# Optimization experiments

Hardware: AMD Instinct MI355X
Metric: run time of the kernel (lower is better)

The kernel has to match this reference:

```python
import jax, jax.numpy as jnp
import numpy as np

B, S, D, H = 1, 2048, 2048, 32
HD = D // H  # head_dim = 64
FF = 4 * D
EPS = 1e-5


def _alibi_slopes(n_heads):
    # standard ALiBi slopes for power-of-2 head counts: 2^(-8i/n)
    return np.array([2.0 ** (-8.0 * (i + 1) / n_heads) for i in range(n_heads)], np.float32)


def setup_inputs() -> dict:
    key = jax.random.key(0)
    ks = jax.random.split(key, 16)
    s = 0.02
    x = jax.random.normal(ks[0], (B, S, D), jnp.float32)
    # alibi bias [B, H, 1, S], broadcast over query positions (HF views alibi as (b, h, 1, kv_len))
    slopes = _alibi_slopes(H)
    alibi_np = slopes[:, None, None] * np.arange(S, dtype=np.float32)[None, None, :]
    alibi = jnp.broadcast_to(jnp.asarray(alibi_np), (B, H, 1, S))
    # additive causal mask [1, 1, S, S]
    causal = np.tril(np.ones((S, S), bool))
    attention_mask = jnp.asarray(np.where(causal, 0.0, -1e9).astype(np.float32))[None, None]
    p = lambda k, shp: s * jax.random.normal(k, shp, jnp.float32)
    return {
        "x": x,
        "alibi": alibi,
        "attention_mask": attention_mask,
        "ln1_g": jnp.ones((D,), jnp.float32), "ln1_b": jnp.zeros((D,), jnp.float32),
        "ln2_g": jnp.ones((D,), jnp.float32), "ln2_b": jnp.zeros((D,), jnp.float32),
        "wqkv": p(ks[1], (D, 3 * D)), "bqkv": jnp.zeros((3 * D,), jnp.float32),
        "wo": p(ks[2], (D, D)), "bo": jnp.zeros((D,), jnp.float32),
        "w1": p(ks[3], (D, FF)), "b1": jnp.zeros((FF,), jnp.float32),
        "w2": p(ks[4], (FF, D)), "b2": jnp.zeros((D,), jnp.float32),
    }


def _layernorm(h, g, b):
    m = h.mean(-1, keepdims=True)
    v = ((h - m) ** 2).mean(-1, keepdims=True)
    return (h - m) * jax.lax.rsqrt(v + EPS) * g + b


def reference(x, alibi, attention_mask, ln1_g, ln1_b, ln2_g, ln2_b,
              wqkv, bqkv, wo, bo, w1, b1, w2, b2):
    b, s, d = x.shape
    inv_norm = 1.0 / np.sqrt(HD).astype(np.float32)
    # --- input layernorm ---
    h = _layernorm(x, ln1_g, ln1_b)
    # --- fused QKV ---
    qkv = h @ wqkv + bqkv
    q, k, v = jnp.split(qkv, 3, axis=-1)
    q = q.reshape(b, s, H, HD).transpose(0, 2, 1, 3)  # [b, h, s, hd]
    k = k.reshape(b, s, H, HD).transpose(0, 2, 1, 3)
    v = v.reshape(b, s, H, HD).transpose(0, 2, 1, 3)
    # --- ALiBi-biased attention (HF falcon alibi path) ---
    scores = jnp.einsum("bhqd,bhkd->bhqk", q, k)          # [b, h, s, s]
    logits = (scores + alibi) * inv_norm + attention_mask  # alibi broadcasts over q dim
    probs = jax.nn.softmax(logits, axis=-1)
    ctx = jnp.einsum("bhqk,bhkd->bhqd", probs, v)
    ctx = ctx.transpose(0, 2, 1, 3).reshape(b, s, d)
    attn_out = ctx @ wo + bo
    # --- residual, post-attn layernorm, MLP (non-parallel falcon-rw layout) ---
    res = x + attn_out
    h2 = _layernorm(res, ln2_g, ln2_b)
    mlp = jax.nn.gelu(h2 @ w1 + b1, approximate=False) @ w2 + b2
    return res + mlp
```

## Files before the change

### kernel.cpp

```cpp
#include <hip/hip_runtime.h>
#include <hip/hip_bf16.h>
#include <cstdint>
#include <cstddef>

static constexpr int Sq  = 2048;
static constexpr int Dm  = 2048;
static constexpr int NH  = 32;
static constexpr int HDm = 64;
static constexpr int FFm = 8192;

typedef __bf16 bf16x8 __attribute__((ext_vector_type(8)));
typedef float  f32x4  __attribute__((ext_vector_type(4)));

__device__ __forceinline__ void async_ld16(const void* g, void* l) {
  __builtin_amdgcn_global_load_lds((const __attribute__((address_space(1))) void*)g,
                                   (__attribute__((address_space(3))) void*)l, 16, 0, 0);
}

__global__ __launch_bounds__(256)
void tcast_kernel(const float* __restrict__ in, __hip_bfloat16* __restrict__ out,
                  int K, int N) {
  __shared__ float tile[64][65];
  const int tc = blockIdx.x * 64;
  const int tr = blockIdx.y * 64;
  const int cx = threadIdx.x & 63;
  const int ry = threadIdx.x >> 6;
#pragma unroll
  for (int i = 0; i < 16; ++i) {
    int r = ry + i * 4;
    tile[r][cx] = in[(size_t)(tr + r) * N + tc + cx];
  }
  __syncthreads();
#pragma unroll
  for (int i = 0; i < 16; ++i) {
    int r = ry + i * 4;
    out[(size_t)(tc + r) * K + tr + cx] = __float2bfloat16(tile[cx][r]);
  }
}

__global__ __launch_bounds__(256)
void ln_kernel(const float* __restrict__ x, const float* __restrict__ g,
               const float* __restrict__ b, __hip_bfloat16* __restrict__ out) {
  __shared__ float red[4];
  const int t = threadIdx.x;
  const float* xr = x + (size_t)blockIdx.x * Dm;
  float v[8];
  float s = 0.f;
#pragma unroll
  for (int i = 0; i < 8; ++i) { v[i] = xr[t + i * 256]; s += v[i]; }
#pragma unroll
  for (int off = 32; off > 0; off >>= 1) s += __shfl_down(s, off, 64);
  if ((t & 63) == 0) red[t >> 6] = s;
  __syncthreads();
  const float mean = (red[0] + red[1] + red[2] + red[3]) * (1.f / Dm);
  __syncthreads();
  float vs = 0.f;
#pragma unroll
  for (int i = 0; i < 8; ++i) { float d = v[i] - mean; vs += d * d; }
#pragma unroll
  for (int off = 32; off > 0; off >>= 1) vs += __shfl_down(vs, off, 64);
  if ((t & 63) == 0) red[t >> 6] = vs;
  __syncthreads();
  const float inv = rsqrtf((red[0] + red[1] + red[2] + red[3]) * (1.f / Dm) + 1e-5f);
  __hip_bfloat16* orow = out + (size_t)blockIdx.x * Dm;
#pragma unroll
  for (int i = 0; i < 8; ++i) {
    int c = t + i * 256;
    orow[c] = __float2bfloat16((v[i] - mean) * inv * g[c] + b[c]);
  }
}

template <int EPI>
__global__ __launch_bounds__(256)
void gemm_kernel(const __hip_bfloat16* __restrict__ A,
                 const __hip_bfloat16* __restrict__ Bt,
                 int N, int K, int Ksub,
                 const float* __restrict__ bias,
                 const float* __restrict__ addsrc,
                 float* __restrict__ outf,
                 __hip_bfloat16* __restrict__ outb,
                 __hip_bfloat16* __restrict__ qo,
                 __hip_bfloat16* __restrict__ ko,
                 __hip_bfloat16* __restrict__ vo,
                 __hip_bfloat16* __restrict__ po) {
  __shared__ __align__(16) __hip_bfloat16 As[2][128 * 32];
  __shared__ __align__(16) __hip_bfloat16 Bs[2][128 * 32];
  const int t = threadIdx.x;
  const int lane = t & 63, w = t >> 6, quad = lane >> 4, l16 = lane & 15;
  const int bn = blockIdx.x, bm = blockIdx.y, bz = blockIdx.z;
  const int wm = (w & 1) * 64, wn = (w >> 1) * 64;
  const __hip_bfloat16* Abase = A + (size_t)bm * 128 * K;
  const __hip_bfloat16* Bbase = Bt + (size_t)bn * 128 * K;
  const int kBeg = bz * Ksub, kEnd = kBeg + Ksub;

  auto stage = [&](int b, int k0) {
#pragma unroll
    for (int j = 0; j < 2; ++j) {
      int c = j * 256 + t;
      int row = c >> 2;
      int p = c & 3;
      int g = (p - (row >> 1)) & 3;
      async_ld16(Abase + (size_t)row * K + k0 + g * 8, &As[b][c * 8]);
      async_ld16(Bbase + (size_t)row * K + k0 + g * 8, &Bs[b][c * 8]);
    }
  };

  f32x4 acc[4][4] = {};
  stage(0, kBeg);
  int buf = 0;
  for (int k0 = kBeg; k0 < kEnd; k0 += 32, buf ^= 1) {
    __syncthreads();
    if (k0 + 32 < kEnd) stage(buf ^ 1, k0 + 32);
    bf16x8 af[4], bfv[4];
#pragma unroll
    for (int i = 0; i < 4; ++i) {
      int row = wm + i * 16 + l16;
      int p = (quad + (row >> 1)) & 3;
      af[i] = *(const bf16x8*)(&As[buf][row * 32 + p * 8]);
    }
#pragma unroll
    for (int i = 0; i < 4; ++i) {
      int row = wn + i * 16 + l16;
      int p = (quad + (row >> 1)) & 3;
      bfv[i] = *(const bf16x8*)(&Bs[buf][row * 32 + p * 8]);
    }
#pragma unroll
    for (int mt = 0; mt < 4; ++mt)
#pragma unroll
      for (int nt = 0; nt < 4; ++nt)
        acc[mt][nt] = __builtin_amdgcn_mfma_f32_16x16x32_bf16(af[mt], bfv[nt], acc[mt][nt], 0, 0, 0);
  }
#pragma unroll
  for (int mt = 0; mt < 4; ++mt) {
#pragma unroll
    for (int nt = 0; nt < 4; ++nt) {
      const int n = bn * 128 + wn + nt * 16 + l16;
      const float bz2 = bias[n];
#pragma unroll
      for (int r = 0; r < 4; ++r) {
        const int m = bm * 128 + wm + mt * 16 + quad * 4 + r;
        float val = acc[mt][nt][r];
        if constexpr (EPI == 0) {
          val += bz2;
          int which = n >> 11, d2 = n & 2047;
          int hh = d2 >> 6, hd = d2 & 63;
          if (which == 0)
            qo[((size_t)hh * Sq + m) * HDm + hd] = __float2bfloat16(val * 0.125f);
          else if (which == 1)
            ko[((size_t)hh * Sq + m) * HDm + hd] = __float2bfloat16(val);
          else
            vo[((size_t)hh * HDm + hd) * Sq + m] = __float2bfloat16(val);
        } else if constexpr (EPI == 1) {
          outf[(size_t)m * N + n] = addsrc[(size_t)m * N + n] + bz2 + val;
        } else if constexpr (EPI == 2) {
          val += bz2;
          float gg = 0.5f * val * (1.0f + erff(val * 0.70710678118654752f));
          outb[(size_t)m * N + n] = __float2bfloat16(gg);
        } else {
          if (bz == 0)
            outf[(size_t)m * N + n] = addsrc[(size_t)m * N + n] + bz2 + val;
          else
            po[(size_t)m * N + n] = __float2bfloat16(val);
        }
      }
    }
  }
}

__global__ __launch_bounds__(256)
void addp_kernel(float* __restrict__ out, const __hip_bfloat16* __restrict__ p) {
  const int i = (blockIdx.x * 256 + threadIdx.x) * 4;
  float4 o = *(const float4*)(out + i);
  const __hip_bfloat16* pp = p + i;
  o.x += (float)pp[0]; o.y += (float)pp[1]; o.z += (float)pp[2]; o.w += (float)pp[3];
  *(float4*)(out + i) = o;
}

__global__ __launch_bounds__(256)
void attn_kernel(const __hip_bfloat16* __restrict__ qb,
                 const __hip_bfloat16* __restrict__ kb,
                 const __hip_bfloat16* __restrict__ vt,
                 const float* __restrict__ alibi,
                 __hip_bfloat16* __restrict__ ctx) {
  __shared__ __align__(16) __hip_bfloat16 Kl[64 * 64];
  __shared__ __align__(16) __hip_bfloat16 Vl[64 * 64];
  __shared__ __align__(16) __hip_bfloat16 Pl[4][16 * 64];
  const int qblk = blockIdx.x, h = blockIdx.y;
  const int t = threadIdx.x, w = t >> 6, lane = t & 63, quad = lane >> 4, l16 = lane & 15;
  const __hip_bfloat16* qh = qb + (size_t)h * Sq * HDm;
  const __hip_bfloat16* kh = kb + (size_t)h * Sq * HDm;
  const __hip_bfloat16* vh = vt + (size_t)h * HDm * Sq;
  const float* al = alibi + (size_t)h * Sq;
  const int qr0 = qblk * 64 + w * 16;
  const bf16x8 qa0 = *(const bf16x8*)(qh + (size_t)(qr0 + l16) * HDm + quad * 8);
  const bf16x8 qa1 = *(const bf16x8*)(qh + (size_t)(qr0 + l16) * HDm + 32 + quad * 8);
  f32x4 o[4] = {};
  float m_i[4], l_i[4];
#pragma unroll
  for (int r = 0; r < 4; ++r) { m_i[r] = -3e38f; l_i[r] = 0.f; }
  for (int kbk = 0; kbk <= qblk; ++kbk) {
    __syncthreads();
#pragma unroll
    for (int j = 0; j < 2; ++j) {
      int c = j * 256 + t;
      int row = c >> 3;
      int swz = (c & 7) ^ (row & 7);
      async_ld16(kh + (size_t)(kbk * 64 + row) * HDm + swz * 8, Kl + c * 8);
      async_ld16(vh + (size_t)row * Sq + kbk * 64 + swz * 8, Vl + c * 8);
    }
    __syncthreads();
    f32x4 sf[4];
    const f32x4 zero = {};
#pragma unroll
    for (int nt = 0; nt < 4; ++nt) {
      int row = nt * 16 + l16;
      bf16x8 kf0 = *(const bf16x8*)(Kl + row * 64 + ((quad ^ (row & 7)) << 3));
      bf16x8 kf1 = *(const bf16x8*)(Kl + row * 64 + (((4 + quad) ^ (row & 7)) << 3));
      sf[nt] = __builtin_amdgcn_mfma_f32_16x16x32_bf16(qa0, kf0, zero, 0, 0, 0);
      sf[nt] = __builtin_amdgcn_mfma_f32_16x16x32_bf16(qa1, kf1, sf[nt], 0, 0, 0);
    }
    const bool diag = (kbk == qblk);
    float mrow[4] = {-3e38f, -3e38f, -3e38f, -3e38f};
#pragma unroll
    for (int nt = 0; nt < 4; ++nt) {
      const float ab = al[kbk * 64 + nt * 16 + l16] * 0.125f;
      const int kcol = nt * 16 + l16;
#pragma unroll
      for (int r = 0; r < 4; ++r) {
        float vv = sf[nt][r] + ab;
        if (diag && kcol > w * 16 + quad * 4 + r) vv = -3e38f;
        sf[nt][r] = vv;
        mrow[r] = fmaxf(mrow[r], vv);
      }
    }
#pragma unroll
    for (int off = 8; off > 0; off >>= 1)
#pragma unroll
      for (int r = 0; r < 4; ++r)
        mrow[r] = fmaxf(mrow[r], __shfl_xor(mrow[r], off, 64));
    float alpha[4], rs[4], p[4][4];
#pragma unroll
    for (int r = 0; r < 4; ++r) {
      float mn = fmaxf(m_i[r], mrow[r]);
      alpha[r] = __expf(m_i[r] - mn);
      m_i[r] = mn;
    }
#pragma unroll
    for (int nt = 0; nt < 4; ++nt)
#pragma unroll
      for (int r = 0; r < 4; ++r) p[nt][r] = __expf(sf[nt][r] - m_i[r]);
#pragma unroll
    for (int r = 0; r < 4; ++r) rs[r] = p[0][r] + p[1][r] + p[2][r] + p[3][r];
#pragma unroll
    for (int off = 8; off > 0; off >>= 1)
#pragma unroll
      for (int r = 0; r < 4; ++r) rs[r] += __shfl_xor(rs[r], off, 64);
#pragma unroll
    for (int r = 0; r < 4; ++r) l_i[r] = l_i[r] * alpha[r] + rs[r];
#pragma unroll
    for (int dt = 0; dt < 4; ++dt)
#pragma unroll
      for (int r = 0; r < 4; ++r) o[dt][r] *= alpha[r];
    __hip_bfloat16* pw = &Pl[w][0];
#pragma unroll
    for (int nt = 0; nt < 4; ++nt)
#pragma unroll
      for (int r = 0; r < 4; ++r) {
        int prow = quad * 4 + r;
        int e = nt * 16 + l16;
        int c16 = e >> 3;
        pw[prow * 64 + ((c16 ^ (prow & 7)) << 3) + (e & 7)] = __float2bfloat16(p[nt][r]);
      }
    asm volatile("s_waitcnt lgkmcnt(0)" ::: "memory");
    const bf16x8 pa0 = *(const bf16x8*)(pw + l16 * 64 + ((quad ^ (l16 & 7)) << 3));
    const bf16x8 pa1 = *(const bf16x8*)(pw + l16 * 64 + (((4 + quad) ^ (l16 & 7)) << 3));
#pragma unroll
    for (int dt = 0; dt < 4; ++dt) {
      int row = dt * 16 + l16;
      bf16x8 v0 = *(const bf16x8*)(Vl + row * 64 + ((quad ^ (row & 7)) << 3));
      bf16x8 v1 = *(const bf16x8*)(Vl + row * 64 + (((4 + quad) ^ (row & 7)) << 3));
      o[dt] = __builtin_amdgcn_mfma_f32_16x16x32_bf16(pa0, v0, o[dt], 0, 0, 0);
      o[dt] = __builtin_amdgcn_mfma_f32_16x16x32_bf16(pa1, v1, o[dt], 0, 0, 0);
    }
  }
#pragma unroll
  for (int dt = 0; dt < 4; ++dt)
#pragma unroll
    for (int r = 0; r < 4; ++r) {
      int srow = qblk * 64 + w * 16 + quad * 4 + r;
      ctx[(size_t)srow * Dm + h * HDm + dt * 16 + l16] =
          __float2bfloat16(o[dt][r] / l_i[r]);
    }
}

extern "C" void kernel_launch(void* const* d_in, const int* in_sizes, int n_in,
                              void* d_out, int out_size, void* d_ws, size_t ws_size,
                              hipStream_t stream) {
  const float* x     = (const float*)d_in[0];
  const float* alibi = (const float*)d_in[1];
  const float* ln1g  = (const float*)d_in[3];
  const float* ln1b  = (const float*)d_in[4];
  const float* ln2g  = (const float*)d_in[5];
  const float* ln2b  = (const float*)d_in[6];
  const float* wqkv  = (const float*)d_in[7];
  const float* bqkv  = (const float*)d_in[8];
  const float* wo    = (const float*)d_in[9];
  const float* bo    = (const float*)d_in[10];
  const float* w1    = (const float*)d_in[11];
  const float* b1    = (const float*)d_in[12];
  const float* w2    = (const float*)d_in[13];
  const float* b2    = (const float*)d_in[14];
  float* out = (float*)d_out;

  char* p = (char*)d_ws;
  auto alloc = [&](size_t bytes) {
    char* r = p;
    p += (bytes + 255) & ~(size_t)255;
    return r;
  };
  constexpr size_t SD2 = (size_t)Sq * Dm * 2;
  char* R2 = alloc((size_t)FFm * Dm * 2);
  char* R1 = alloc(4 * SD2);
  __hip_bfloat16* hb   = (__hip_bfloat16*)alloc(SD2);
  float*          resb = (float*)alloc((size_t)Sq * Dm * 4);

  __hip_bfloat16* wqkvT = (__hip_bfloat16*)R2;
  __hip_bfloat16* w1T   = (__hip_bfloat16*)R2;
  __hip_bfloat16* w2T   = (__hip_bfloat16*)R2;
  __hip_bfloat16* qbuf  = (__hip_bfloat16*)(R1 + 0 * SD2);
  __hip_bfloat16* kbuf  = (__hip_bfloat16*)(R1 + 1 * SD2);
  __hip_bfloat16* vtbuf = (__hip_bfloat16*)(R1 + 2 * SD2);
  __hip_bfloat16* ctxb  = (__hip_bfloat16*)(R1 + 3 * SD2);
  __hip_bfloat16* woT   = (__hip_bfloat16*)(R1 + 0 * SD2);
  __hip_bfloat16* t1b   = (__hip_bfloat16*)R1;
  __hip_bfloat16* part  = hb;

  tcast_kernel<<<dim3(3 * Dm / 64, Dm / 64), 256, 0, stream>>>(wqkv, wqkvT, Dm, 3 * Dm);
  ln_kernel<<<Sq, 256, 0, stream>>>(x, ln1g, ln1b, hb);
  gemm_kernel<0><<<dim3(3 * Dm / 128, Sq / 128), 256, 0, stream>>>(
      hb, wqkvT, 3 * Dm, Dm, Dm, bqkv, nullptr, nullptr, nullptr, qbuf, kbuf, vtbuf, nullptr);
  tcast_kernel<<<dim3(FFm / 64, Dm / 64), 256, 0, stream>>>(w1, w1T, Dm, FFm);
  attn_kernel<<<dim3(Sq / 64, NH), 256, 0, stream>>>(qbuf, kbuf, vtbuf, alibi, ctxb);
  tcast_kernel<<<dim3(Dm / 64, Dm / 64), 256, 0, stream>>>(wo, woT, Dm, Dm);
  gemm_kernel<1><<<dim3(Dm / 128, Sq / 128), 256, 0, stream>>>(
      ctxb, woT, Dm, Dm, Dm, bo, x, resb, nullptr, nullptr, nullptr, nullptr, nullptr);
  ln_kernel<<<Sq, 256, 0, stream>>>(resb, ln2g, ln2b, hb);
  gemm_kernel<2><<<dim3(FFm / 128, Sq / 128), 256, 0, stream>>>(
      hb, w1T, FFm, Dm, Dm, b1, nullptr, nullptr, t1b, nullptr, nullptr, nullptr, nullptr);
  tcast_kernel<<<dim3(Dm / 64, FFm / 64), 256, 0, stream>>>(w2, w2T, FFm, Dm);
  gemm_kernel<3><<<dim3(Dm / 128, Sq / 128, 2), 256, 0, stream>>>(
      t1b, w2T, Dm, FFm, FFm / 2, b2, resb, out, nullptr, nullptr, nullptr, nullptr, part);
  addp_kernel<<<(Sq * Dm) / 1024, 256, 0, stream>>>(out, part);
}
```

Baseline: 715.5 us.

## Pair causal query blocks per attention CTA, double-buffer K/V, split-K output projection

Each attention block now handles two query blocks, one from the front and one from the back of the sequence, so every CTA does the same amount of causal work and the grid is halved. K/V tiles are double-buffered so the next tile's async loads overlap the current tile's compute. The Wo projection switches to the split-K GEMM variant with a partial buffer plus an add pass, for more parallelism. This costs twice the LDS for K/V, an extra kernel launch, and relies on gemm_kernel<3>'s epilogue correctly handling bias and residual for this projection.

```diff
diff --git a/kernel.cpp b/kernel.cpp
--- a/kernel.cpp
+++ b/kernel.cpp
@@ -182,42 +182,62 @@
                  const __hip_bfloat16* __restrict__ vt,
                  const float* __restrict__ alibi,
                  __hip_bfloat16* __restrict__ ctx) {
-  __shared__ __align__(16) __hip_bfloat16 Kl[64 * 64];
-  __shared__ __align__(16) __hip_bfloat16 Vl[64 * 64];
+  __shared__ __align__(16) __hip_bfloat16 Kl[2][64 * 64];
+  __shared__ __align__(16) __hip_bfloat16 Vl[2][64 * 64];
   __shared__ __align__(16) __hip_bfloat16 Pl[4][16 * 64];
-  const int qblk = blockIdx.x, h = blockIdx.y;
+  const int pi = blockIdx.x, h = blockIdx.y;
+  const int qA = pi, qB = (Sq / 64 - 1) - pi;
   const int t = threadIdx.x, w = t >> 6, lane = t & 63, quad = lane >> 4, l16 = lane & 15;
   const __hip_bfloat16* qh = qb + (size_t)h * Sq * HDm;
   const __hip_bfloat16* kh = kb + (size_t)h * Sq * HDm;
   const __hip_bfloat16* vh = vt + (size_t)h * HDm * Sq;
   const float* al = alibi + (size_t)h * Sq;
-  const int qr0 = qblk * 64 + w * 16;
-  const bf16x8 qa0 = *(const bf16x8*)(qh + (size_t)(qr0 + l16) * HDm + quad * 8);
-  const bf16x8 qa1 = *(const bf16x8*)(qh + (size_t)(qr0 + l16) * HDm + 32 + quad * 8);
-  f32x4 o[4] = {};
-  float m_i[4], l_i[4];
-#pragma unroll
-  for (int r = 0; r < 4; ++r) { m_i[r] = -3e38f; l_i[r] = 0.f; }
-  for (int kbk = 0; kbk <= qblk; ++kbk) {
-    __syncthreads();
+
+  const int rA = qA * 64 + w * 16 + l16;
+  const int rB = qB * 64 + w * 16 + l16;
+  const bf16x8 qA0 = *(const bf16x8*)(qh + (size_t)rA * HDm + quad * 8);
+  const bf16x8 qA1 = *(const bf16x8*)(qh + (size_t)rA * HDm + 32 + quad * 8);
+  const bf16x8 qB0 = *(const bf16x8*)(qh + (size_t)rB * HDm + quad * 8);
+  const bf16x8 qB1 = *(const bf16x8*)(qh + (size_t)rB * HDm + 32 + quad * 8);
+
+  auto stageS = [&](int b, int s) {
+    const int kbk = (s <= qA) ? s : s - qA - 1;
 #pragma unroll
     for (int j = 0; j < 2; ++j) {
       int c = j * 256 + t;
       int row = c >> 3;
       int swz = (c & 7) ^ (row & 7);
-      async_ld16(kh + (size_t)(kbk * 64 + row) * HDm + swz * 8, Kl + c * 8);
-      async_ld16(vh + (size_t)row * Sq + kbk * 64 + swz * 8, Vl + c * 8);
-    }
+      async_ld16(kh + (size_t)(kbk * 64 + row) * HDm + swz * 8, &Kl[b][c * 8]);
+      async_ld16(vh + (size_t)row * Sq + kbk * 64 + swz * 8, &Vl[b][c * 8]);
+    }
+  };
+
+  f32x4 o[4] = {};
+  float m_i[4], l_i[4];
+#pragma unroll
+  for (int r = 0; r < 4; ++r) { m_i[r] = -3e38f; l_i[r] = 0.f; }
+
+  const int total = qA + qB + 2;
+  stageS(0, 0);
+  int buf = 0;
+  for (int s = 0; s < total; ++s, buf ^= 1) {
     __syncthreads();
+    if (s + 1 < total) stageS(buf ^ 1, s + 1);
+    const bool ph = (s > qA);
+    const int kbk = ph ? s - qA - 1 : s;
+    const int qblk = ph ? qB : qA;
+    const bf16x8 a0 = ph ? qB0 : qA0;
+    const bf16x8 a1 = ph ? qB1 : qA1;
+
     f32x4 sf[4];
     const f32x4 zero = {};
 #pragma unroll
     for (int nt = 0; nt < 4; ++nt) {
       int row = nt * 16 + l16;
-      bf16x8 kf0 = *(const bf16x8*)(Kl + row * 64 + ((quad ^ (row & 7)) << 3));
-      bf16x8 kf1 = *(const bf16x8*)(Kl + row * 64 + (((4 + quad) ^ (row & 7)) << 3));
-      sf[nt] = __builtin_amdgcn_mfma_f32_16x16x32_bf16(qa0, kf0, zero, 0, 0, 0);
-      sf[nt] = __builtin_amdgcn_mfma_f32_16x16x32_bf16(qa1, kf1, sf[nt], 0, 0, 0);
+      bf16x8 kf0 = *(const bf16x8*)(&Kl[buf][row * 64 + ((quad ^ (row & 7)) << 3)]);
+      bf16x8 kf1 = *(const bf16x8*)(&Kl[buf][row * 64 + (((4 + quad) ^ (row & 7)) << 3)]);
+      sf[nt] = __builtin_amdgcn_mfma_f32_16x16x32_bf16(a0, kf0, zero, 0, 0, 0);
+      sf[nt] = __builtin_amdgcn_mfma_f32_16x16x32_bf16(a1, kf1, sf[nt], 0, 0, 0);
     }
     const bool diag = (kbk == qblk);
     float mrow[4] = {-3e38f, -3e38f, -3e38f, -3e38f};
@@ -277,17 +297,30 @@
 #pragma unroll
     for (int dt = 0; dt < 4; ++dt) {
       int row = dt * 16 + l16;
-      bf16x8 v0 = *(const bf16x8*)(Vl + row * 64 + ((quad ^ (row & 7)) << 3));
-      bf16x8 v1 = *(const bf16x8*)(Vl + row * 64 + (((4 + quad) ^ (row & 7)) << 3));
+      bf16x8 v0 = *(const bf16x8*)(&Vl[buf][row * 64 + ((quad ^ (row & 7)) << 3)]);
+      bf16x8 v1 = *(const bf16x8*)(&Vl[buf][row * 64 + (((4 + quad) ^ (row & 7)) << 3)]);
       o[dt] = __builtin_amdgcn_mfma_f32_16x16x32_bf16(pa0, v0, o[dt], 0, 0, 0);
       o[dt] = __builtin_amdgcn_mfma_f32_16x16x32_bf16(pa1, v1, o[dt], 0, 0, 0);
     }
+    if (s == qA) {
+#pragma unroll
+      for (int dt = 0; dt < 4; ++dt)
+#pragma unroll
+        for (int r = 0; r < 4; ++r) {
+          int srow = qA * 64 + w * 16 + quad * 4 + r;
+          ctx[(size_t)srow * Dm + h * HDm + dt * 16 + l16] =
+              __float2bfloat16(o[dt][r] / l_i[r]);
+          o[dt][r] = 0.f;
+        }
+#pragma unroll
+      for (int r = 0; r < 4; ++r) { m_i[r] = -3e38f; l_i[r] = 0.f; }
+    }
   }
 #pragma unroll
   for (int dt = 0; dt < 4; ++dt)
 #pragma unroll
     for (int r = 0; r < 4; ++r) {
-      int srow = qblk * 64 + w * 16 + quad * 4 + r;
+      int srow = qB * 64 + w * 16 + quad * 4 + r;
       ctx[(size_t)srow * Dm + h * HDm + dt * 16 + l16] =
           __float2bfloat16(o[dt][r] / l_i[r]);
     }
@@ -340,10 +373,11 @@
   gemm_kernel<0><<<dim3(3 * Dm / 128, Sq / 128), 256, 0, stream>>>(
       hb, wqkvT, 3 * Dm, Dm, Dm, bqkv, nullptr, nullptr, nullptr, qbuf, kbuf, vtbuf, nullptr);
   tcast_kernel<<<dim3(FFm / 64, Dm / 64), 256, 0, stream>>>(w1, w1T, Dm, FFm);
-  attn_kernel<<<dim3(Sq / 64, NH), 256, 0, stream>>>(qbuf, kbuf, vtbuf, alibi, ctxb);
+  attn_kernel<<<dim3(Sq / 128, NH), 256, 0, stream>>>(qbuf, kbuf, vtbuf, alibi, ctxb);
   tcast_kernel<<<dim3(Dm / 64, Dm / 64), 256, 0, stream>>>(wo, woT, Dm, Dm);
-  gemm_kernel<1><<<dim3(Dm / 128, Sq / 128), 256, 0, stream>>>(
-      ctxb, woT, Dm, Dm, Dm, bo, x, resb, nullptr, nullptr, nullptr, nullptr, nullptr);
+  gemm_kernel<3><<<dim3(Dm / 128, Sq / 128, 2), 256, 0, stream>>>(
+      ctxb, woT, Dm, Dm, Dm / 2, bo, x, resb, nullptr, nullptr, nullptr, nullptr, part);
+  addp_kernel<<<(Sq * Dm) / 1024, 256, 0, stream>>>(resb, part);
   ln_kernel<<<Sq, 256, 0, stream>>>(resb, ln2g, ln2b, hb);
   gemm_kernel<2><<<dim3(FFm / 128, Sq / 128), 256, 0, stream>>>(
       hb, w1T, FFm, Dm, Dm, b1, nullptr, nullptr, t1b, nullptr, nullptr, nullptr, nullptr);
```

Result: faster. 674.6 us (-5.7%).
